# Kernel optimization log

Hardware: AMD Instinct MI355X
Metric: run time of the kernel (lower is better)

## Reference

```python
import jax, jax.numpy as jnp
import numpy as np

N_EMBD = 1024
N_HEAD = 16
HEAD_DIM = N_EMBD // N_HEAD


def setup_inputs() -> dict:
    key = jax.random.key(0)
    kx, kq, kk, kv, ko = jax.random.split(key, 5)
    s = 1.0 / np.sqrt(N_EMBD)
    return {
        "x": jax.random.normal(kx, (4, 2048, N_EMBD), dtype=jnp.float32),
        "Wq": jax.random.normal(kq, (N_EMBD, N_EMBD), dtype=jnp.float32) * s,
        "Wk": jax.random.normal(kk, (N_EMBD, N_EMBD), dtype=jnp.float32) * s,
        "Wv": jax.random.normal(kv, (N_EMBD, N_EMBD), dtype=jnp.float32) * s,
        "Wo": jax.random.normal(ko, (N_EMBD, N_EMBD), dtype=jnp.float32) * s,
    }


def reference(x, Wq, Wk, Wv, Wo):
    B, T, C = x.shape
    H, D = N_HEAD, HEAD_DIM
    # projections; torch Linear computes x @ W.T
    q = (x @ Wq.T).reshape(B, T, H, D).transpose(0, 2, 1, 3)  # [B,H,T,D]
    k = (x @ Wk.T).reshape(B, T, H, D).transpose(0, 2, 1, 3)
    v = (x @ Wv.T).reshape(B, T, H, D).transpose(0, 2, 1, 3)
    scores = jnp.einsum("bhtd,bhsd->bhts", q, k) / np.sqrt(D).astype(np.float32)
    causal = jnp.tril(jnp.ones((T, T), dtype=bool))
    scores = jnp.where(causal, scores, -jnp.inf)
    attn = jax.nn.softmax(scores, axis=-1)
    out = jnp.einsum("bhts,bhsd->bhtd", attn, v)  # [B,H,T,D]
    out = out.transpose(0, 2, 1, 3).reshape(B, T, C)
    return out @ Wo.T
```

## Files before the change

### kernel.cpp

```cpp
#include <hip/hip_runtime.h>
#include <hip/hip_bf16.h>


typedef __bf16 bf16_t;
typedef __bf16 bf16x4 __attribute__((ext_vector_type(4)));
typedef __bf16 bf16x8 __attribute__((ext_vector_type(8)));
typedef float  f32x4  __attribute__((ext_vector_type(4)));

#define MFMA16(a, b, c) __builtin_amdgcn_mfma_f32_16x16x32_bf16(a, b, c, 0, 0, 0)

__device__ __forceinline__ float exp2_(float x) {
#if __has_builtin(__builtin_amdgcn_exp2f)
    return __builtin_amdgcn_exp2f(x);
#else
    return __expf(x * 0.6931471805599453f);
#endif
}

__device__ __forceinline__ void gload_lds16(const bf16_t* g, bf16_t* l) {
    __builtin_amdgcn_global_load_lds(
        (const __attribute__((address_space(1))) void*)g,
        (__attribute__((address_space(3))) void*)l, 16, 0, 0);
}

__global__ __launch_bounds__(256)
void cast_f32_bf16(const float* __restrict__ in, bf16_t* __restrict__ out, int n8) {
    int i = blockIdx.x * 256 + threadIdx.x;
    if (i >= n8) return;
    const float4* p = (const float4*)in;
    float4 a = p[i * 2], b = p[i * 2 + 1];
    bf16x8 o;
    o[0] = (bf16_t)a.x; o[1] = (bf16_t)a.y; o[2] = (bf16_t)a.z; o[3] = (bf16_t)a.w;
    o[4] = (bf16_t)b.x; o[5] = (bf16_t)b.y; o[6] = (bf16_t)b.z; o[7] = (bf16_t)b.w;
    *(bf16x8*)(out + (size_t)i * 8) = o;
}

__global__ __launch_bounds__(256)
void cast4_f32_bf16(const float* __restrict__ i0, const float* __restrict__ i1,
                    const float* __restrict__ i2, const float* __restrict__ i3,
                    bf16_t* o0, bf16_t* o1, bf16_t* o2, bf16_t* o3, int n8) {
    const float* in = blockIdx.y == 0 ? i0 : blockIdx.y == 1 ? i1 : blockIdx.y == 2 ? i2 : i3;
    bf16_t*     out = blockIdx.y == 0 ? o0 : blockIdx.y == 1 ? o1 : blockIdx.y == 2 ? o2 : o3;
    int i = blockIdx.x * 256 + threadIdx.x;
    if (i >= n8) return;
    const float4* p = (const float4*)in;
    float4 a = p[i * 2], b = p[i * 2 + 1];
    bf16x8 o;
    o[0] = (bf16_t)a.x; o[1] = (bf16_t)a.y; o[2] = (bf16_t)a.z; o[3] = (bf16_t)a.w;
    o[4] = (bf16_t)b.x; o[5] = (bf16_t)b.y; o[6] = (bf16_t)b.z; o[7] = (bf16_t)b.w;
    *(bf16x8*)(out + (size_t)i * 8) = o;
}

template<int OUT_BF16>
__global__ __launch_bounds__(256)
void gemm_bt(const bf16_t* __restrict__ A, const bf16_t* __restrict__ B,
             void* __restrict__ Cv, int M, int N, int K) {
    __shared__ bf16_t As[128 * 32];
    __shared__ bf16_t Bs[128 * 32];
    const int tid = threadIdx.x;
    const int lane = tid & 63;
    const int w = tid >> 6;
    const int wm = w >> 1, wn = w & 1;
    const int g = lane >> 4, c = lane & 15;
    const long bm = (long)blockIdx.x * 128;
    const long bn = (long)blockIdx.y * 128;

    f32x4 acc[4][4] = {};

    const int srow = tid >> 2;
    const int scol = (tid & 3) << 3;
    const bf16_t* Ag = A + (bm + srow) * (long)K + scol;
    const bf16_t* Bg = B + (bn + srow) * (long)K + scol;
    bf16_t* AsW = As + tid * 8;
    bf16_t* BsW = Bs + tid * 8;

    for (int k0 = 0; k0 < K; k0 += 32) {
        gload_lds16(Ag + k0,                 AsW);
        gload_lds16(Ag + k0 + (long)64 * K,  AsW + 2048);
        gload_lds16(Bg + k0,                 BsW);
        gload_lds16(Bg + k0 + (long)64 * K,  BsW + 2048);
        __syncthreads();
        bf16x8 af[4], bfr[4];
        #pragma unroll
        for (int m = 0; m < 4; ++m)
            af[m] = *(const bf16x8*)(As + (wm * 64 + m * 16 + c) * 32 + g * 8);
        #pragma unroll
        for (int n = 0; n < 4; ++n)
            bfr[n] = *(const bf16x8*)(Bs + (wn * 64 + n * 16 + c) * 32 + g * 8);
        #pragma unroll
        for (int m = 0; m < 4; ++m)
            #pragma unroll
            for (int n = 0; n < 4; ++n)
                acc[m][n] = MFMA16(af[m], bfr[n], acc[m][n]);
        __syncthreads();
    }
    #pragma unroll
    for (int m = 0; m < 4; ++m)
        #pragma unroll
        for (int n = 0; n < 4; ++n)
            #pragma unroll
            for (int i = 0; i < 4; ++i) {
                long row = bm + wm * 64 + m * 16 + g * 4 + i;
                long col = bn + wn * 64 + n * 16 + c;
                float v = acc[m][n][i];
                if (OUT_BF16) ((bf16_t*)Cv)[row * N + col] = (bf16_t)v;
                else          ((float*)Cv)[row * N + col]  = v;
            }
}


__device__ __forceinline__ void stage_K(const bf16_t* Kp, long rowb, int kb, int hcol,
                                        bf16_t* Kbuf, int tid) {
    int row = tid >> 3;
    int lb  = (tid & 7) ^ (row & 7);
    gload_lds16(Kp + (rowb + kb + row) * 3072 + hcol + lb * 8, Kbuf + tid * 8);
}

__device__ __forceinline__ void load_V(const bf16_t* Vp, long rowb, int kb, int hcol,
                                       int tid, unsigned int* vr) {
    const int d0 = (tid & 31) * 2;
    const int k0 = (tid >> 5) * 4;
    const unsigned int* src =
        (const unsigned int*)(Vp + (rowb + kb + k0) * 3072 + hcol + d0);
    #pragma unroll
    for (int i = 0; i < 4; ++i) vr[i] = src[(size_t)i * 1536];
}

__device__ __forceinline__ void write_Vt(bf16_t* Vbuf, int tid, const unsigned int* vr) {
    const int d0 = (tid & 31) * 2;
    const int k0 = (tid >> 5) * 4;
    unsigned int lo[2], hi[2];
    #pragma unroll
    for (int i = 0; i < 2; ++i) {
        lo[i] = (vr[2 * i] & 0xffffu) | (vr[2 * i + 1] << 16);
        hi[i] = (vr[2 * i] >> 16)     | (vr[2 * i + 1] & 0xffff0000u);
    }
    *(uint2*)&Vbuf[(d0 + 0) * 72 + k0] = make_uint2(lo[0], lo[1]);
    *(uint2*)&Vbuf[(d0 + 1) * 72 + k0] = make_uint2(hi[0], hi[1]);
}

__global__ __launch_bounds__(512, 4)
void attn_kernel(const bf16_t* __restrict__ Qp, const bf16_t* __restrict__ Kp,
                 const bf16_t* __restrict__ Vp, bf16_t* __restrict__ O) {
    __shared__ bf16_t Ks[2][64 * 64];
    __shared__ bf16_t Vts[2][64 * 72];
    __shared__ bf16_t PW[8][16 * 72];

    const int tid = threadIdx.x, lane = tid & 63, w = tid >> 6;
    const int g = lane >> 4, c = lane & 15;
    const int bh = blockIdx.x, bx = blockIdx.y;
    const int b = bh >> 4, h = bh & 15;
    const long rowb = (long)b * 2048;
    const int hcol = h * 64;
    const float QSCL = 0.18033688011112042f;

    for (int pass = 0; pass < 2; ++pass) {
        const int q0  = pass ? (15 - bx) : bx;
        const int qlo = q0 * 128 + w * 16;
        const int nkt = 2 * q0 + 2;

        bf16x8 qf[2];
        #pragma unroll
        for (int ks = 0; ks < 2; ++ks) {
            qf[ks] = *(const bf16x8*)(Qp + (rowb + qlo + c) * 3072 +
                                      hcol + ks * 32 + g * 8);
            #pragma unroll
            for (int j = 0; j < 8; ++j)
                qf[ks][j] = (bf16_t)((float)qf[ks][j] * QSCL);
        }

        float m_r = -1e30f, l_r = 0.f;
        f32x4 acc[4] = {};

        stage_K(Kp, rowb, 0, hcol, Ks[0], tid);
        {
            unsigned int vr0[4];
            load_V(Vp, rowb, 0, hcol, tid, vr0);
            write_Vt(Vts[0], tid, vr0);
        }
        __syncthreads();

        for (int t = 0; t < nkt; ++t) {
            const int cur = t & 1;
            const int kb = t * 64;
            const bool pre = (t + 1 < nkt);
            unsigned int vr[4];
            if (pre) {
                stage_K(Kp, rowb, kb + 64, hcol, Ks[cur ^ 1], tid);
                load_V(Vp, rowb, kb + 64, hcol, tid, vr);
            }

            if (kb <= qlo + 15) {
                f32x4 sacc[4] = {};
                #pragma unroll
                for (int nt = 0; nt < 4; ++nt) {
                    const int row = nt * 16 + c;
                    #pragma unroll
                    for (int ks = 0; ks < 2; ++ks) {
                        bf16x8 kf = *(const bf16x8*)&Ks[cur][row * 64 +
                                        (((ks * 4 + g) ^ (c & 7)) * 8)];
                        sacc[nt] = MFMA16(kf, qf[ks], sacc[nt]);
                    }
                }
                if (kb + 63 > qlo) {
                    const int q = qlo + c;
                    #pragma unroll
                    for (int nt = 0; nt < 4; ++nt)
                        #pragma unroll
                        for (int i = 0; i < 4; ++i) {
                            int key = kb + nt * 16 + g * 4 + i;
                            if (key > q) sacc[nt][i] = -1e30f;
                        }
                }

                float mx = sacc[0][0];
                #pragma unroll
                for (int nt = 0; nt < 4; ++nt)
                    #pragma unroll
                    for (int i = 0; i < 4; ++i)
                        mx = fmaxf(mx, sacc[nt][i]);
                mx = fmaxf(mx, __shfl_xor(mx, 16, 64));
                mx = fmaxf(mx, __shfl_xor(mx, 32, 64));
                if (__any(mx > m_r + 8.f)) {
                    float mnew = fmaxf(m_r, mx);
                    float scl = exp2_(m_r - mnew);
                    #pragma unroll
                    for (int nt = 0; nt < 4; ++nt)
                        acc[nt] *= scl;
                    l_r *= scl;
                    m_r = mnew;
                }
                float rs = 0.f;
                #pragma unroll
                for (int nt = 0; nt < 4; ++nt)
                    #pragma unroll
                    for (int i = 0; i < 4; ++i) {
                        float pv = exp2_(sacc[nt][i] - m_r);
                        sacc[nt][i] = pv;
                        rs += pv;
                    }
                rs += __shfl_xor(rs, 16, 64);
                rs += __shfl_xor(rs, 32, 64);
                l_r += rs;

                #pragma unroll
                for (int nt = 0; nt < 4; ++nt) {
                    bf16x4 t4;
                    #pragma unroll
                    for (int i = 0; i < 4; ++i) t4[i] = (bf16_t)sacc[nt][i];
                    *(bf16x4*)&PW[w][c * 72 + nt * 16 + g * 4] = t4;
                }

                #pragma unroll
                for (int ks = 0; ks < 2; ++ks) {
                    bf16x8 pf = *(const bf16x8*)&PW[w][c * 72 + ks * 32 + g * 8];
                    #pragma unroll
                    for (int nt = 0; nt < 4; ++nt) {
                        bf16x8 vf = *(const bf16x8*)&Vts[cur][(nt * 16 + c) * 72 +
                                                              ks * 32 + g * 8];
                        acc[nt] = MFMA16(vf, pf, acc[nt]);
                    }
                }
            }

            if (pre) write_Vt(Vts[cur ^ 1], tid, vr);
            __syncthreads();
        }

        {
            float rl = __builtin_amdgcn_rcpf(l_r);
            #pragma unroll
            for (int nt = 0; nt < 4; ++nt) {
                bf16x4 t4;
                #pragma unroll
                for (int i = 0; i < 4; ++i) t4[i] = (bf16_t)(acc[nt][i] * rl);
                *(bf16x4*)&PW[w][c * 72 + nt * 16 + g * 4] = t4;
            }
        }
        #pragma unroll
        for (int p = 0; p < 2; ++p) {
            int row = p * 8 + (lane >> 3);
            int ch  = (lane & 7) * 8;
            bf16x8 v = *(const bf16x8*)&PW[w][row * 72 + ch];
            *(bf16x8*)&O[(rowb + qlo + row) * 1024 + hcol + ch] = v;
        }
    }
}

extern "C" void kernel_launch(void* const* d_in, const int* in_sizes, int n_in,
                              void* d_out, int out_size, void* d_ws, size_t ws_size,
                              hipStream_t stream) {
    const float* x  = (const float*)d_in[0];
    const float* Wq = (const float*)d_in[1];
    const float* Wk = (const float*)d_in[2];
    const float* Wv = (const float*)d_in[3];
    const float* Wo = (const float*)d_in[4];

    const int M = 8192;
    const int C = 1024;

    char* ws = (char*)d_ws;
    bf16_t* xb   = (bf16_t*)(ws);
    bf16_t* wqkv = (bf16_t*)(ws + ((size_t)16 << 20));
    bf16_t* wob  = (bf16_t*)(ws + ((size_t)22 << 20));
    bf16_t* qkv  = (bf16_t*)(ws + ((size_t)24 << 20));
    bf16_t* aob  = (bf16_t*)(ws + ((size_t)72 << 20));

    cast_f32_bf16<<<(M * C / 8) / 256, 256, 0, stream>>>(x, xb, M * C / 8);
    cast4_f32_bf16<<<dim3((C * C / 8) / 256, 4), 256, 0, stream>>>(
        Wq, Wk, Wv, Wo,
        wqkv, wqkv + (size_t)(C * C), wqkv + (size_t)(2 * C * C), wob, C * C / 8);

    gemm_bt<1><<<dim3(M / 128, 3072 / 128), 256, 0, stream>>>(xb, wqkv, qkv, M, 3072, C);

    attn_kernel<<<dim3(64, 8), 512, 0, stream>>>(
        qkv, qkv + 1024, qkv + 2048, aob);

    gemm_bt<0><<<dim3(M / 128, C / 128), 256, 0, stream>>>(aob, wob, d_out, M, C, C);
}
```

Before: 187.9 us.

## Swizzle GEMM block order, simplify V transpose, add setprio and tree reductions

The GEMM grid is remapped so consecutive workgroups are spread across eight chunks, aiming for better cache locality across dies. The V tile is now loaded as eight scalar bf16 reads per thread and written as one 16-byte LDS store, replacing the packed 32-bit shuffle transpose. s_setprio is raised around the MFMA sections of attention, and the max and sum reductions are rewritten as balanced trees to shorten dependency chains. The scalar 2-byte global loads for V may coalesce worse than the previous 4-byte loads.

```diff
diff --git a/kernel.cpp b/kernel.cpp
--- a/kernel.cpp
+++ b/kernel.cpp
@@ -62,8 +62,13 @@
     const int w = tid >> 6;
     const int wm = w >> 1, wn = w & 1;
     const int g = lane >> 4, c = lane & 15;
-    const long bm = (long)blockIdx.x * 128;
-    const long bn = (long)blockIdx.y * 128;
+
+    const int gx = gridDim.x;
+    const int lin = blockIdx.x + gx * blockIdx.y;
+    const int chunk = (gx * gridDim.y) >> 3;
+    const int nlin = (lin & 7) * chunk + (lin >> 3);
+    const long bm = (long)(nlin % gx) * 128;
+    const long bn = (long)(nlin / gx) * 128;
 
     f32x4 acc[4][4] = {};
 
@@ -116,27 +121,21 @@
     gload_lds16(Kp + (rowb + kb + row) * 3072 + hcol + lb * 8, Kbuf + tid * 8);
 }
 
-__device__ __forceinline__ void load_V(const bf16_t* Vp, long rowb, int kb, int hcol,
-                                       int tid, unsigned int* vr) {
-    const int d0 = (tid & 31) * 2;
-    const int k0 = (tid >> 5) * 4;
-    const unsigned int* src =
-        (const unsigned int*)(Vp + (rowb + kb + k0) * 3072 + hcol + d0);
+__device__ __forceinline__ bf16x8 load_V8(const bf16_t* Vp, long rowb, int kb,
+                                          int hcol, int tid) {
+    const int d  = tid & 63;
+    const int k0 = (tid >> 6) * 8;
+    bf16x8 v;
     #pragma unroll
-    for (int i = 0; i < 4; ++i) vr[i] = src[(size_t)i * 1536];
-}
-
-__device__ __forceinline__ void write_Vt(bf16_t* Vbuf, int tid, const unsigned int* vr) {
-    const int d0 = (tid & 31) * 2;
-    const int k0 = (tid >> 5) * 4;
-    unsigned int lo[2], hi[2];
-    #pragma unroll
-    for (int i = 0; i < 2; ++i) {
-        lo[i] = (vr[2 * i] & 0xffffu) | (vr[2 * i + 1] << 16);
-        hi[i] = (vr[2 * i] >> 16)     | (vr[2 * i + 1] & 0xffff0000u);
-    }
-    *(uint2*)&Vbuf[(d0 + 0) * 72 + k0] = make_uint2(lo[0], lo[1]);
-    *(uint2*)&Vbuf[(d0 + 1) * 72 + k0] = make_uint2(hi[0], hi[1]);
+    for (int j = 0; j < 8; ++j)
+        v[j] = Vp[(rowb + kb + k0 + j) * 3072 + hcol + d];
+    return v;
+}
+
+__device__ __forceinline__ void write_V8(bf16_t* Vbuf, int tid, bf16x8 v) {
+    const int d  = tid & 63;
+    const int k0 = (tid >> 6) * 8;
+    *(bf16x8*)&Vbuf[d * 72 + k0] = v;
 }
 
 __global__ __launch_bounds__(512, 4)
@@ -173,25 +172,22 @@
         f32x4 acc[4] = {};
 
         stage_K(Kp, rowb, 0, hcol, Ks[0], tid);
-        {
-            unsigned int vr0[4];
-            load_V(Vp, rowb, 0, hcol, tid, vr0);
-            write_Vt(Vts[0], tid, vr0);
-        }
+        write_V8(Vts[0], tid, load_V8(Vp, rowb, 0, hcol, tid));
         __syncthreads();
 
         for (int t = 0; t < nkt; ++t) {
             const int cur = t & 1;
             const int kb = t * 64;
             const bool pre = (t + 1 < nkt);
-            unsigned int vr[4];
+            bf16x8 vreg;
             if (pre) {
                 stage_K(Kp, rowb, kb + 64, hcol, Ks[cur ^ 1], tid);
-                load_V(Vp, rowb, kb + 64, hcol, tid, vr);
+                vreg = load_V8(Vp, rowb, kb + 64, hcol, tid);
             }
 
             if (kb <= qlo + 15) {
                 f32x4 sacc[4] = {};
+                __builtin_amdgcn_s_setprio(1);
                 #pragma unroll
                 for (int nt = 0; nt < 4; ++nt) {
                     const int row = nt * 16 + c;
@@ -202,6 +198,7 @@
                         sacc[nt] = MFMA16(kf, qf[ks], sacc[nt]);
                     }
                 }
+                __builtin_amdgcn_s_setprio(0);
                 if (kb + 63 > qlo) {
                     const int q = qlo + c;
                     #pragma unroll
@@ -213,12 +210,16 @@
                         }
                 }
 
-                float mx = sacc[0][0];
-                #pragma unroll
-                for (int nt = 0; nt < 4; ++nt)
-                    #pragma unroll
-                    for (int i = 0; i < 4; ++i)
-                        mx = fmaxf(mx, sacc[nt][i]);
+                float mx01a = fmaxf(sacc[0][0], sacc[0][1]);
+                float mx01b = fmaxf(sacc[0][2], sacc[0][3]);
+                float mx11a = fmaxf(sacc[1][0], sacc[1][1]);
+                float mx11b = fmaxf(sacc[1][2], sacc[1][3]);
+                float mx21a = fmaxf(sacc[2][0], sacc[2][1]);
+                float mx21b = fmaxf(sacc[2][2], sacc[2][3]);
+                float mx31a = fmaxf(sacc[3][0], sacc[3][1]);
+                float mx31b = fmaxf(sacc[3][2], sacc[3][3]);
+                float mx = fmaxf(fmaxf(fmaxf(mx01a, mx01b), fmaxf(mx11a, mx11b)),
+                                 fmaxf(fmaxf(mx21a, mx21b), fmaxf(mx31a, mx31b)));
                 mx = fmaxf(mx, __shfl_xor(mx, 16, 64));
                 mx = fmaxf(mx, __shfl_xor(mx, 32, 64));
                 if (__any(mx > m_r + 8.f)) {
@@ -230,15 +231,15 @@
                     l_r *= scl;
                     m_r = mnew;
                 }
-                float rs = 0.f;
-                #pragma unroll
-                for (int nt = 0; nt < 4; ++nt)
-                    #pragma unroll
-                    for (int i = 0; i < 4; ++i) {
-                        float pv = exp2_(sacc[nt][i] - m_r);
-                        sacc[nt][i] = pv;
-                        rs += pv;
-                    }
+                float rsn[4];
+                #pragma unroll
+                for (int nt = 0; nt < 4; ++nt) {
+                    #pragma unroll
+                    for (int i = 0; i < 4; ++i)
+                        sacc[nt][i] = exp2_(sacc[nt][i] - m_r);
+                    rsn[nt] = (sacc[nt][0] + sacc[nt][1]) + (sacc[nt][2] + sacc[nt][3]);
+                }
+                float rs = (rsn[0] + rsn[1]) + (rsn[2] + rsn[3]);
                 rs += __shfl_xor(rs, 16, 64);
                 rs += __shfl_xor(rs, 32, 64);
                 l_r += rs;
@@ -251,6 +252,7 @@
                     *(bf16x4*)&PW[w][c * 72 + nt * 16 + g * 4] = t4;
                 }
 
+                __builtin_amdgcn_s_setprio(1);
                 #pragma unroll
                 for (int ks = 0; ks < 2; ++ks) {
                     bf16x8 pf = *(const bf16x8*)&PW[w][c * 72 + ks * 32 + g * 8];
@@ -261,9 +263,10 @@
                         acc[nt] = MFMA16(vf, pf, acc[nt]);
                     }
                 }
+                __builtin_amdgcn_s_setprio(0);
             }
 
-            if (pre) write_Vt(Vts[cur ^ 1], tid, vr);
+            if (pre) write_V8(Vts[cur ^ 1], tid, vreg);
             __syncthreads();
         }
 
```

Measured after the change: 194.6 us. 3.6% more time.
